# Kernel tuning notes

Hardware: AMD Instinct MI355X
Metric: run time of the kernel (lower is better)

## Reference

```python
import jax, jax.numpy as jnp
import numpy as np

B, L, D, H = 2, 256, 512, 8
DV = D // H
INF = 1e12

def _xavier(key, shape, fan_in, fan_out):
    a = float(np.sqrt(6.0 / (fan_in + fan_out)))
    return jax.random.uniform(key, shape, minval=-a, maxval=a, dtype=jnp.float32)

def setup_inputs() -> dict:
    key = jax.random.key(0)
    ks = jax.random.split(key, 9)
    inp = jax.random.normal(ks[0], (B, L, D), dtype=jnp.float32)
    relation_inp = jax.random.normal(ks[1], (B, L, L, D), dtype=jnp.float32)
    mask = jax.random.randint(ks[2], (B, L, L), 0, 2).astype(bool)
    adj_mask = jax.random.randint(ks[3], (B, H, L, L), 0, 2).astype(jnp.float32)
    W_value = _xavier(ks[4], (D, H * DV), D, H * DV)
    W_relation = _xavier(ks[5], (D, H * DV), D, H * DV)
    # weight vectors have torch shape (1,1,1,H,DV); xavier fans over last two dims
    w_src = _xavier(ks[6], (H, DV), H, DV)
    w_tgt = _xavier(ks[7], (H, DV), H, DV)
    w_rel = _xavier(ks[8], (H, DV), H, DV)
    return {"inp": inp, "relation_inp": relation_inp, "mask": mask,
            "adj_mask": adj_mask, "W_value": W_value, "W_relation": W_relation,
            "w_src": w_src, "w_tgt": w_tgt, "w_rel": w_rel}

def reference(inp, relation_inp, mask, adj_mask, W_value, W_relation, w_src, w_tgt, w_rel):
    b, l, d = inp.shape
    h, dv = w_src.shape
    # value: (B,H,L,DV)
    value = (inp @ W_value).reshape(b, l, h, dv).transpose(0, 2, 1, 3)
    # relation: (B,L,L,H,DV)
    relation = (relation_inp @ W_relation).reshape(b, l, l, h, dv)
    # scores[b,h,i,j] = w_src.v_j + w_tgt.v_i + w_rel.rel[b,i,j,h]
    s_src = jnp.einsum('bhjd,hd->bhj', value, w_src)[:, :, None, :]
    s_tgt = jnp.einsum('bhid,hd->bhi', value, w_tgt)[:, :, :, None]
    s_rel = jnp.einsum('bijhd,hd->bhij', relation, w_rel)
    scores = s_src + s_tgt + s_rel
    scores = jnp.where(scores >= 0, scores, 0.2 * scores)  # LeakyReLU(0.2)
    m = mask[:, None]  # (B,1,L,L)
    adj_zero = adj_mask == 0
    scores = jnp.where(m, -INF, scores)
    scores = jnp.where(adj_zero, -INF, scores)
    attn = jax.nn.softmax(scores, axis=-1)
    # normalized: divide by edge weight (zeros -> weight INF -> 1/INF)
    inv = jnp.where(adj_zero, 1.0 / INF, 1.0 / jnp.where(adj_zero, 1.0, adj_mask))
    attn = attn * inv
    attn = attn / jnp.maximum(jnp.sum(jnp.abs(attn), axis=-1, keepdims=True), 1e-12)
    attn = jnp.where(m, 0.0, attn)
    attn = jnp.where(adj_zero, 0.0, attn)
    out = jnp.einsum('bhij,bhjd->bhid', attn, value)
    out = out.transpose(0, 2, 1, 3).reshape(b, l, d)  # concat heads
    return out + inp
```

## Files before the change

### kernel.cpp

```cpp
#include <hip/hip_runtime.h>

#define B_ 2
#define L_ 256
#define D_ 512
#define H_ 8
#define DV_ 64
#define NEGINF 1e12f

#define WS_VALUE 0
#define WS_WR    262144
#define WS_SSRC  266240
#define WS_STGT  270336
#define WS_SREL  274432

__global__ __launch_bounds__(256) void k_wr(const float* __restrict__ Wrel,
                                            const float* __restrict__ wrel,
                                            float* __restrict__ WR) {
    int flat = blockIdx.x * 256 + threadIdx.x;
    int k = flat >> 3, h = flat & 7;
    const float* a = Wrel + k * 512 + h * 64;
    const float* b = wrel + h * 64;
    float s = 0.f;
#pragma unroll
    for (int d = 0; d < 64; d += 4) {
        float4 x = *(const float4*)(a + d);
        float4 y = *(const float4*)(b + d);
        s += x.x * y.x + x.y * y.y + x.z * y.z + x.w * y.w;
    }
    WR[k * 8 + h] = s;
}

__global__ __launch_bounds__(256) void k_value(const float* __restrict__ inp,
                                               const float* __restrict__ Wv,
                                               const float* __restrict__ wsrc,
                                               const float* __restrict__ wtgt,
                                               float* __restrict__ value,
                                               float* __restrict__ s_src,
                                               float* __restrict__ s_tgt) {
    int blk = blockIdx.x;
    int ct  = blk & 1;
    int rt  = blk >> 1;
    int n   = ct * 256 + threadIdx.x;
    int r0  = rt * 4;
    const float* i0 = inp + (size_t)(r0 + 0) * 512;
    const float* i1 = inp + (size_t)(r0 + 1) * 512;
    const float* i2 = inp + (size_t)(r0 + 2) * 512;
    const float* i3 = inp + (size_t)(r0 + 3) * 512;
    float a0 = 0.f, a1 = 0.f, a2 = 0.f, a3 = 0.f;
#pragma unroll 16
    for (int k = 0; k < 512; ++k) {
        float w = Wv[(size_t)k * 512 + n];
        a0 = fmaf(i0[k], w, a0);
        a1 = fmaf(i1[k], w, a1);
        a2 = fmaf(i2[k], w, a2);
        a3 = fmaf(i3[k], w, a3);
    }
    int h = n >> 6, dv = n & 63;
    float acc[4] = {a0, a1, a2, a3};
    float wsv = wsrc[h * 64 + dv];
    float wtv = wtgt[h * 64 + dv];
#pragma unroll
    for (int r = 0; r < 4; ++r) {
        int row = r0 + r;
        int b = row >> 8, l = row & 255;
        value[(((size_t)(b * 8 + h)) * 256 + l) * 64 + dv] = acc[r];
        float ss = acc[r] * wsv;
        float st = acc[r] * wtv;
#pragma unroll
        for (int off = 32; off >= 1; off >>= 1) {
            ss += __shfl_xor(ss, off);
            st += __shfl_xor(st, off);
        }
        if (dv == 0) {
            s_src[(size_t)(b * 8 + h) * 256 + l] = ss;
            s_tgt[(size_t)(b * 8 + h) * 256 + l] = st;
        }
    }
}

__global__ __launch_bounds__(256, 3) void k_srel(const float* __restrict__ rel,
                                                 const float* __restrict__ WR,
                                                 float* __restrict__ srel) {
    int tid  = threadIdx.x;
    int lane = tid & 63;
    int gw   = blockIdx.x * 4 + (tid >> 6);

    float wa[32], wb[32];
    {
        const float4* wp = (const float4*)(WR + 32 * lane);
        const float4* wq = (const float4*)(WR + 2048 + 32 * lane);
#pragma unroll
        for (int s = 0; s < 8; ++s) {
            float4 t = wp[s];
            wa[4 * s] = t.x; wa[4 * s + 1] = t.y; wa[4 * s + 2] = t.z; wa[4 * s + 3] = t.w;
            float4 u = wq[s];
            wb[4 * s] = u.x; wb[4 * s + 1] = u.y; wb[4 * s + 2] = u.z; wb[4 * s + 3] = u.w;
        }
    }

    const float* rp = rel + (size_t)gw * 32 * 512 + lane * 4;

#define LOADLO(j) (*(const float4*)(rp + (size_t)(j) * 512))
#define LOADHI(j) (*(const float4*)(rp + (size_t)(j) * 512 + 256))

#define ROW(lo, hi, jj)                                                        \
    {                                                                          \
        float A[8];                                                            \
        _Pragma("unroll")                                                      \
        for (int h = 0; h < 8; ++h) {                                          \
            A[h] = fmaf(lo.x, wa[h],                                           \
                   fmaf(lo.y, wa[8 + h],                                       \
                   fmaf(lo.z, wa[16 + h],                                      \
                   fmaf(lo.w, wa[24 + h],                                      \
                   fmaf(hi.x, wb[h],                                           \
                   fmaf(hi.y, wb[8 + h],                                       \
                   fmaf(hi.z, wb[16 + h],                                      \
                        hi.w * wb[24 + h])))))));                              \
        }                                                                      \
        _Pragma("unroll")                                                      \
        for (int h = 0; h < 8; ++h) {                                          \
            A[h] += __shfl_xor(A[h], 8);                                       \
            A[h] += __shfl_xor(A[h], 16);                                      \
            A[h] += __shfl_xor(A[h], 32);                                      \
        }                                                                      \
        int hi3 = lane >> 3;                                                   \
        float v = A[0];                                                        \
        _Pragma("unroll")                                                      \
        for (int h = 1; h < 8; ++h) v = (hi3 == h) ? A[h] : v;                 \
        v += __shfl_xor(v, 1);                                                 \
        v += __shfl_xor(v, 2);                                                 \
        v += __shfl_xor(v, 4);                                                 \
        if ((lane & 7) == 0) {                                                 \
            int R = gw * 32 + (jj);                                            \
            srel[((size_t)(R >> 8)) * 2048 + hi3 * 256 + (R & 255)] = v;       \
        }                                                                      \
    }

    float4 loA = LOADLO(0), hiA = LOADHI(0);
    float4 loB = LOADLO(1), hiB = LOADHI(1);
#pragma unroll 1
    for (int jj = 0; jj < 32; jj += 2) {
        float4 nloA, nhiA, nloB, nhiB;
        if (jj + 2 < 32) { nloA = LOADLO(jj + 2); nhiA = LOADHI(jj + 2); }
        if (jj + 3 < 32) { nloB = LOADLO(jj + 3); nhiB = LOADHI(jj + 3); }
        ROW(loA, hiA, jj);
        ROW(loB, hiB, jj + 1);
        loA = nloA; hiA = nhiA; loB = nloB; hiB = nhiB;
    }
#undef ROW
#undef LOADLO
#undef LOADHI
}

__global__ __launch_bounds__(256) void k_attn(const int*   __restrict__ mask,
                                              const float* __restrict__ adj,
                                              const float* __restrict__ inp,
                                              const float* __restrict__ value,
                                              const float* __restrict__ srel,
                                              const float* __restrict__ s_src,
                                              const float* __restrict__ s_tgt,
                                              float* __restrict__ out) {
    __shared__ float attn_s[2048];
    int bi  = blockIdx.x;
    int b   = bi >> 8;
    int i   = bi & 255;
    int tid = threadIdx.x;

    {
        int h  = tid >> 5;
        int ln = tid & 31;
        float stgt = s_tgt[(size_t)(b * 8 + h) * 256 + i];
        const float* ssrc   = s_src + (size_t)(b * 8 + h) * 256;
        const float* srl    = srel + (size_t)bi * 2048 + h * 256;
        const float* adjrow = adj + ((size_t)(b * 8 + h) * 256 + i) * 256;
        const int*   mrow   = mask + (size_t)bi * 256;

        float sc[8], av[8];
        int mb = 0;
        float rowmax = -3.0e38f;
#pragma unroll
        for (int t = 0; t < 8; ++t) {
            int j = ln + 32 * t;
            float a = adjrow[j];
            av[t] = a;
            int m = mrow[j];
            float s = ssrc[j] + stgt + srl[j];
            s = (s >= 0.f) ? s : 0.2f * s;
            if (m != 0) { s = -NEGINF; mb |= (1 << t); }
            if (a == 0.f) s = -NEGINF;
            sc[t] = s;
            rowmax = fmaxf(rowmax, s);
        }
#pragma unroll
        for (int off = 16; off >= 1; off >>= 1)
            rowmax = fmaxf(rowmax, __shfl_xor(rowmax, off));

        float rowsum = 0.f;
#pragma unroll
        for (int t = 0; t < 8; ++t) {
            sc[t] = expf(sc[t] - rowmax);
            rowsum += sc[t];
        }
#pragma unroll
        for (int off = 16; off >= 1; off >>= 1)
            rowsum += __shfl_xor(rowsum, off);
        float rinv = 1.0f / rowsum;

        float sumabs = 0.f;
#pragma unroll
        for (int t = 0; t < 8; ++t) {
            float p = sc[t] * rinv;
            float invv = (av[t] == 0.f) ? 1e-12f : (1.0f / av[t]);
            p *= invv;
            sc[t] = p;
            sumabs += fabsf(p);
        }
#pragma unroll
        for (int off = 16; off >= 1; off >>= 1)
            sumabs += __shfl_xor(sumabs, off);

        float rdn = 1.0f / fmaxf(sumabs, 1e-12f);
#pragma unroll
        for (int t = 0; t < 8; ++t) {
            float p = sc[t] * rdn;
            if (mb & (1 << t)) p = 0.f;
            if (av[t] == 0.f) p = 0.f;
            attn_s[h * 256 + ln + 32 * t] = p;
        }
    }
    __syncthreads();

    {
        int h  = tid >> 5;
        int d0 = (tid & 31) * 2;
        const float* vbase = value + ((size_t)(b * 8 + h) * 256) * 64 + d0;
        const float* arow  = attn_s + h * 256;
        float ax = 0.f, ay = 0.f;
#pragma unroll 8
        for (int j = 0; j < 256; ++j) {
            float a = arow[j];
            float2 v2 = *(const float2*)(vbase + (size_t)j * 64);
            ax = fmaf(a, v2.x, ax);
            ay = fmaf(a, v2.y, ay);
        }
        size_t o = (size_t)bi * 512 + h * 64 + d0;
        out[o]     = inp[o] + ax;
        out[o + 1] = inp[o + 1] + ay;
    }
}

extern "C" void kernel_launch(void* const* d_in, const int* in_sizes, int n_in,
                              void* d_out, int out_size, void* d_ws, size_t ws_size,
                              hipStream_t stream) {
    const float* inp      = (const float*)d_in[0];
    const float* rel      = (const float*)d_in[1];
    const int*   mask     = (const int*)  d_in[2];
    const float* adj      = (const float*)d_in[3];
    const float* W_value  = (const float*)d_in[4];
    const float* W_rel    = (const float*)d_in[5];
    const float* w_src    = (const float*)d_in[6];
    const float* w_tgt    = (const float*)d_in[7];
    const float* w_rel    = (const float*)d_in[8];
    float* out = (float*)d_out;

    float* ws    = (float*)d_ws;
    float* value = ws + WS_VALUE;
    float* WR    = ws + WS_WR;
    float* s_src = ws + WS_SSRC;
    float* s_tgt = ws + WS_STGT;
    float* srel  = ws + WS_SREL;

    k_wr<<<16, 256, 0, stream>>>(W_rel, w_rel, WR);
    k_srel<<<1024, 256, 0, stream>>>(rel, WR, srel);
    k_value<<<256, 256, 0, stream>>>(inp, W_value, w_src, w_tgt,
                                     value, s_src, s_tgt);
    k_attn<<<B_ * L_, 256, 0, stream>>>(mask, adj, inp, value, srel,
                                        s_src, s_tgt, out);
}
```

Before: 125.0 us.

## Compute relation scores with bf16 MFMA instead of FP32 FMA and shuffles

```diff
diff --git a/kernel.cpp b/kernel.cpp
--- a/kernel.cpp
+++ b/kernel.cpp
@@ -9,9 +9,19 @@
 
 #define WS_VALUE 0
 #define WS_WR    262144
-#define WS_SSRC  266240
-#define WS_STGT  270336
-#define WS_SREL  274432
+#define WS_WRFRG 266240
+#define WS_SSRC  270336
+#define WS_STGT  274432
+#define WS_SREL  278528
+
+typedef __attribute__((ext_vector_type(8))) short bf16x8;
+typedef __attribute__((ext_vector_type(4))) float f32x4;
+
+__device__ inline unsigned short f2bf(float f) {
+    unsigned u = __float_as_uint(f);
+    unsigned r = ((u >> 16) & 1) + 0x7FFFu;
+    return (unsigned short)((u + r) >> 16);
+}
 
 __global__ __launch_bounds__(256) void k_wr(const float* __restrict__ Wrel,
                                             const float* __restrict__ wrel,
@@ -28,6 +38,22 @@
         s += x.x * y.x + x.y * y.y + x.z * y.z + x.w * y.w;
     }
     WR[k * 8 + h] = s;
+}
+
+__global__ __launch_bounds__(256) void k_frag(const float* __restrict__ WR,
+                                              unsigned short* __restrict__ WRfrag) {
+    int t = blockIdx.x * 256 + threadIdx.x;
+    int kt = t >> 6, lane = t & 63;
+    int sg = lane >> 4, n = lane & 15;
+    unsigned int w[4];
+#pragma unroll
+    for (int p = 0; p < 4; ++p) {
+        int k0 = kt * 32 + sg * 8 + 2 * p;
+        float v0 = (n < 8) ? WR[k0 * 8 + n] : 0.f;
+        float v1 = (n < 8) ? WR[(k0 + 1) * 8 + n] : 0.f;
+        w[p] = (unsigned)f2bf(v0) | ((unsigned)f2bf(v1) << 16);
+    }
+    *(uint4*)&WRfrag[(size_t)t * 8] = make_uint4(w[0], w[1], w[2], w[3]);
 }
 
 __global__ __launch_bounds__(256) void k_value(const float* __restrict__ inp,
@@ -79,77 +105,42 @@
 }
 
 __global__ __launch_bounds__(256, 3) void k_srel(const float* __restrict__ rel,
-                                                 const float* __restrict__ WR,
+                                                 const unsigned short* __restrict__ WRfrag,
                                                  float* __restrict__ srel) {
     int tid  = threadIdx.x;
+    int wv   = tid >> 6;
     int lane = tid & 63;
-    int gw   = blockIdx.x * 4 + (tid >> 6);
-
-    float wa[32], wb[32];
-    {
-        const float4* wp = (const float4*)(WR + 32 * lane);
-        const float4* wq = (const float4*)(WR + 2048 + 32 * lane);
-#pragma unroll
-        for (int s = 0; s < 8; ++s) {
-            float4 t = wp[s];
-            wa[4 * s] = t.x; wa[4 * s + 1] = t.y; wa[4 * s + 2] = t.z; wa[4 * s + 3] = t.w;
-            float4 u = wq[s];
-            wb[4 * s] = u.x; wb[4 * s + 1] = u.y; wb[4 * s + 2] = u.z; wb[4 * s + 3] = u.w;
-        }
-    }
-
-    const float* rp = rel + (size_t)gw * 32 * 512 + lane * 4;
-
-#define LOADLO(j) (*(const float4*)(rp + (size_t)(j) * 512))
-#define LOADHI(j) (*(const float4*)(rp + (size_t)(j) * 512 + 256))
-
-#define ROW(lo, hi, jj)                                                        \
-    {                                                                          \
-        float A[8];                                                            \
-        _Pragma("unroll")                                                      \
-        for (int h = 0; h < 8; ++h) {                                          \
-            A[h] = fmaf(lo.x, wa[h],                                           \
-                   fmaf(lo.y, wa[8 + h],                                       \
-                   fmaf(lo.z, wa[16 + h],                                      \
-                   fmaf(lo.w, wa[24 + h],                                      \
-                   fmaf(hi.x, wb[h],                                           \
-                   fmaf(hi.y, wb[8 + h],                                       \
-                   fmaf(hi.z, wb[16 + h],                                      \
-                        hi.w * wb[24 + h])))))));                              \
-        }                                                                      \
-        _Pragma("unroll")                                                      \
-        for (int h = 0; h < 8; ++h) {                                          \
-            A[h] += __shfl_xor(A[h], 8);                                       \
-            A[h] += __shfl_xor(A[h], 16);                                      \
-            A[h] += __shfl_xor(A[h], 32);                                      \
-        }                                                                      \
-        int hi3 = lane >> 3;                                                   \
-        float v = A[0];                                                        \
-        _Pragma("unroll")                                                      \
-        for (int h = 1; h < 8; ++h) v = (hi3 == h) ? A[h] : v;                 \
-        v += __shfl_xor(v, 1);                                                 \
-        v += __shfl_xor(v, 2);                                                 \
-        v += __shfl_xor(v, 4);                                                 \
-        if ((lane & 7) == 0) {                                                 \
-            int R = gw * 32 + (jj);                                            \
-            srel[((size_t)(R >> 8)) * 2048 + hi3 * 256 + (R & 255)] = v;       \
-        }                                                                      \
-    }
-
-    float4 loA = LOADLO(0), hiA = LOADHI(0);
-    float4 loB = LOADLO(1), hiB = LOADHI(1);
-#pragma unroll 1
-    for (int jj = 0; jj < 32; jj += 2) {
-        float4 nloA, nhiA, nloB, nhiB;
-        if (jj + 2 < 32) { nloA = LOADLO(jj + 2); nhiA = LOADHI(jj + 2); }
-        if (jj + 3 < 32) { nloB = LOADLO(jj + 3); nhiB = LOADHI(jj + 3); }
-        ROW(loA, hiA, jj);
-        ROW(loB, hiB, jj + 1);
-        loA = nloA; hiA = nhiA; loB = nloB; hiB = nhiB;
-    }
-#undef ROW
-#undef LOADLO
-#undef LOADHI
+    int row0 = blockIdx.x * 64 + wv * 16;
+    int r    = lane & 15;
+    int sg   = lane >> 4;
+
+    bf16x8 bf[16];
+#pragma unroll
+    for (int kt = 0; kt < 16; ++kt)
+        bf[kt] = *(const bf16x8*)&WRfrag[((size_t)kt * 64 + lane) * 8];
+
+    const float* ap = rel + (size_t)(row0 + r) * 512 + sg * 8;
+
+    f32x4 acc = {0.f, 0.f, 0.f, 0.f};
+#pragma unroll 4
+    for (int kt = 0; kt < 16; ++kt) {
+        float4 x0 = *(const float4*)(ap + kt * 32);
+        float4 x1 = *(const float4*)(ap + kt * 32 + 4);
+        bf16x8 a;
+        a[0] = (short)f2bf(x0.x); a[1] = (short)f2bf(x0.y);
+        a[2] = (short)f2bf(x0.z); a[3] = (short)f2bf(x0.w);
+        a[4] = (short)f2bf(x1.x); a[5] = (short)f2bf(x1.y);
+        a[6] = (short)f2bf(x1.z); a[7] = (short)f2bf(x1.w);
+        acc = __builtin_amdgcn_mfma_f32_16x16x32_bf16(a, bf[kt], acc, 0, 0, 0);
+    }
+
+    int n = lane & 15;
+    if (n < 8) {
+        int bi = row0 >> 8;
+        int jb = (row0 & 255) + sg * 4;
+        float* sp = srel + (size_t)bi * 2048 + n * 256 + jb;
+        sp[0] = acc[0]; sp[1] = acc[1]; sp[2] = acc[2]; sp[3] = acc[3];
+    }
 }
 
 __global__ __launch_bounds__(256) void k_attn(const int*   __restrict__ mask,
@@ -263,17 +254,19 @@
     const float* w_rel    = (const float*)d_in[8];
     float* out = (float*)d_out;
 
-    float* ws    = (float*)d_ws;
-    float* value = ws + WS_VALUE;
-    float* WR    = ws + WS_WR;
-    float* s_src = ws + WS_SSRC;
-    float* s_tgt = ws + WS_STGT;
-    float* srel  = ws + WS_SREL;
+    float* ws               = (float*)d_ws;
+    float* value            = ws + WS_VALUE;
+    float* WR               = ws + WS_WR;
+    unsigned short* WRfrag  = (unsigned short*)(ws + WS_WRFRG);
+    float* s_src            = ws + WS_SSRC;
+    float* s_tgt            = ws + WS_STGT;
+    float* srel             = ws + WS_SREL;
 
     k_wr<<<16, 256, 0, stream>>>(W_rel, w_rel, WR);
-    k_srel<<<1024, 256, 0, stream>>>(rel, WR, srel);
+    k_frag<<<4, 256, 0, stream>>>(WR, WRfrag);
     k_value<<<256, 256, 0, stream>>>(inp, W_value, w_src, w_tgt,
                                      value, s_src, s_tgt);
+    k_srel<<<2048, 256, 0, stream>>>(rel, WRfrag, srel);
     k_attn<<<B_ * L_, 256, 0, stream>>>(mask, adj, inp, value, srel,
                                         s_src, s_tgt, out);
 }
```

Result: slower. 158.0 us (+26.4%).

## Skip relation rows for masked pairs and restructure srel reduction via shared memory

Applied to the files above, without the earlier changes.

```diff
diff --git a/kernel.cpp b/kernel.cpp
--- a/kernel.cpp
+++ b/kernel.cpp
@@ -78,78 +78,70 @@
     }
 }
 
-__global__ __launch_bounds__(256, 3) void k_srel(const float* __restrict__ rel,
+__global__ __launch_bounds__(512, 4) void k_srel(const float* __restrict__ rel,
+                                                 const int*   __restrict__ mask,
                                                  const float* __restrict__ WR,
                                                  float* __restrict__ srel) {
-    int tid  = threadIdx.x;
-    int lane = tid & 63;
-    int gw   = blockIdx.x * 4 + (tid >> 6);
-
-    float wa[32], wb[32];
+    __shared__ float red[128 * 16 * 8];
+    int t     = threadIdx.x;
+    int blk   = blockIdx.x;
+    int grow0 = blk * 16;
+    int c     = t & 127;
+    int rg    = t >> 7;
+
+    float wr[32];
     {
-        const float4* wp = (const float4*)(WR + 32 * lane);
-        const float4* wq = (const float4*)(WR + 2048 + 32 * lane);
+        const float4* wp = (const float4*)(WR + (size_t)c * 32);
 #pragma unroll
         for (int s = 0; s < 8; ++s) {
-            float4 t = wp[s];
-            wa[4 * s] = t.x; wa[4 * s + 1] = t.y; wa[4 * s + 2] = t.z; wa[4 * s + 3] = t.w;
-            float4 u = wq[s];
-            wb[4 * s] = u.x; wb[4 * s + 1] = u.y; wb[4 * s + 2] = u.z; wb[4 * s + 3] = u.w;
-        }
-    }
-
-    const float* rp = rel + (size_t)gw * 32 * 512 + lane * 4;
-
-#define LOADLO(j) (*(const float4*)(rp + (size_t)(j) * 512))
-#define LOADHI(j) (*(const float4*)(rp + (size_t)(j) * 512 + 256))
-
-#define ROW(lo, hi, jj)                                                        \
-    {                                                                          \
-        float A[8];                                                            \
-        _Pragma("unroll")                                                      \
-        for (int h = 0; h < 8; ++h) {                                          \
-            A[h] = fmaf(lo.x, wa[h],                                           \
-                   fmaf(lo.y, wa[8 + h],                                       \
-                   fmaf(lo.z, wa[16 + h],                                      \
-                   fmaf(lo.w, wa[24 + h],                                      \
-                   fmaf(hi.x, wb[h],                                           \
-                   fmaf(hi.y, wb[8 + h],                                       \
-                   fmaf(hi.z, wb[16 + h],                                      \
-                        hi.w * wb[24 + h])))))));                              \
-        }                                                                      \
-        _Pragma("unroll")                                                      \
-        for (int h = 0; h < 8; ++h) {                                          \
-            A[h] += __shfl_xor(A[h], 8);                                       \
-            A[h] += __shfl_xor(A[h], 16);                                      \
-            A[h] += __shfl_xor(A[h], 32);                                      \
-        }                                                                      \
-        int hi3 = lane >> 3;                                                   \
-        float v = A[0];                                                        \
-        _Pragma("unroll")                                                      \
-        for (int h = 1; h < 8; ++h) v = (hi3 == h) ? A[h] : v;                 \
-        v += __shfl_xor(v, 1);                                                 \
-        v += __shfl_xor(v, 2);                                                 \
-        v += __shfl_xor(v, 4);                                                 \
-        if ((lane & 7) == 0) {                                                 \
-            int R = gw * 32 + (jj);                                            \
-            srel[((size_t)(R >> 8)) * 2048 + hi3 * 256 + (R & 255)] = v;       \
-        }                                                                      \
-    }
-
-    float4 loA = LOADLO(0), hiA = LOADHI(0);
-    float4 loB = LOADLO(1), hiB = LOADHI(1);
-#pragma unroll 1
-    for (int jj = 0; jj < 32; jj += 2) {
-        float4 nloA, nhiA, nloB, nhiB;
-        if (jj + 2 < 32) { nloA = LOADLO(jj + 2); nhiA = LOADHI(jj + 2); }
-        if (jj + 3 < 32) { nloB = LOADLO(jj + 3); nhiB = LOADHI(jj + 3); }
-        ROW(loA, hiA, jj);
-        ROW(loB, hiB, jj + 1);
-        loA = nloA; hiA = nhiA; loB = nloB; hiB = nhiB;
-    }
-#undef ROW
-#undef LOADLO
-#undef LOADHI
+            float4 v = wp[s];
+            wr[4 * s] = v.x; wr[4 * s + 1] = v.y;
+            wr[4 * s + 2] = v.z; wr[4 * s + 3] = v.w;
+        }
+    }
+
+    const float4* rb   = (const float4*)rel + (size_t)blk * 2048;
+    const int*    mrow = mask + grow0;
+
+    float acc[4][8];
+#pragma unroll
+    for (int p = 0; p < 4; ++p)
+#pragma unroll
+        for (int h = 0; h < 8; ++h) acc[p][h] = 0.f;
+
+#pragma unroll
+    for (int p = 0; p < 4; ++p) {
+        int rl = p * 4 + rg;
+        if (mrow[rl] == 0) {
+            float4 x = rb[p * 512 + t];
+#pragma unroll
+            for (int h = 0; h < 8; ++h) {
+                acc[p][h] = fmaf(x.x, wr[h],
+                            fmaf(x.y, wr[8 + h],
+                            fmaf(x.z, wr[16 + h],
+                            fmaf(x.w, wr[24 + h], acc[p][h]))));
+            }
+        }
+    }
+
+#pragma unroll
+    for (int p = 0; p < 4; ++p) {
+        int rl = p * 4 + rg;
+        float* dst = &red[((size_t)c * 16 + rl) * 8];
+        *(float4*)dst       = make_float4(acc[p][0], acc[p][1], acc[p][2], acc[p][3]);
+        *(float4*)(dst + 4) = make_float4(acc[p][4], acc[p][5], acc[p][6], acc[p][7]);
+    }
+    __syncthreads();
+
+    if (t < 128) {
+        int r = t >> 3, h = t & 7;
+        float s = 0.f;
+#pragma unroll 16
+        for (int c2 = 0; c2 < 128; ++c2)
+            s += red[((size_t)c2 * 16 + r) * 8 + h];
+        int R = grow0 + r;
+        srel[((size_t)(R >> 8)) * 2048 + h * 256 + (R & 255)] = s;
+    }
 }
 
 __global__ __launch_bounds__(256) void k_attn(const int*   __restrict__ mask,
@@ -271,9 +263,9 @@
     float* srel  = ws + WS_SREL;
 
     k_wr<<<16, 256, 0, stream>>>(W_rel, w_rel, WR);
-    k_srel<<<1024, 256, 0, stream>>>(rel, WR, srel);
     k_value<<<256, 256, 0, stream>>>(inp, W_value, w_src, w_tgt,
                                      value, s_src, s_tgt);
+    k_srel<<<8192, 512, 0, stream>>>(rel, mask, WR, srel);
     k_attn<<<B_ * L_, 256, 0, stream>>>(mask, adj, inp, value, srel,
                                         s_src, s_tgt, out);
 }
```

Result: slower. 204.6 us (+63.7%).
